# Kernel tuning notes

Measured on AMD Instinct MI355X. Metric: run time of the kernel, lower is better.

Reference implementation:

```python
import jax, jax.numpy as jnp
import numpy as np

N = 100000      # nodes
E = 3200000     # edges (avg degree 32)
F_IN = 512      # input features
H = 16          # hidden (module default)
C = 40          # classes


def _linear_params(key, fan_in, fan_out):
    # torch.nn.Linear default init: U(-1/sqrt(fan_in), 1/sqrt(fan_in))
    k1, k2 = jax.random.split(key)
    lim = 1.0 / np.sqrt(fan_in)
    W = jax.random.uniform(k1, (fan_in, fan_out), jnp.float32, -lim, lim)
    b = jax.random.uniform(k2, (fan_out,), jnp.float32, -lim, lim)
    return W, b


def setup_inputs() -> dict:
    key = jax.random.key(0)
    ks = jax.random.split(key, 8)
    x = jax.random.normal(ks[0], (N, F_IN), jnp.float32)
    edge_index = jax.random.randint(ks[1], (2, E), 0, N, dtype=jnp.int64)
    edge_weight = jax.random.uniform(ks[2], (E,), jnp.float32)
    W_first, b_first = _linear_params(ks[3], F_IN, H)
    W_conv1, b_conv1 = _linear_params(ks[4], H, H)
    W_conv2, b_conv2 = _linear_params(ks[5], H, H)
    W_out, b_out = _linear_params(ks[6], H, C)
    return {
        "x": x, "edge_index": edge_index, "edge_weight": edge_weight,
        "W_first": W_first, "b_first": b_first,
        "W_conv1": W_conv1, "b_conv1": b_conv1,
        "W_conv2": W_conv2, "b_conv2": b_conv2,
        "W_out": W_out, "b_out": b_out,
    }


def _gcn_conv(x, W, b, row, col, ew):
    # PyG GCNConv: h = x @ W; out_i = sum_{(j->i)} norm_e * h_j + b
    # norm_e = deg^-1/2[row] * w_e * deg^-1/2[col], deg from target (col) index,
    # with self-loops (weight 1) already appended to row/col/ew.
    n = x.shape[0]
    deg = jax.ops.segment_sum(ew, col, num_segments=n)
    dinv = jnp.where(deg > 0, jax.lax.rsqrt(deg), 0.0)
    norm = dinv[row] * ew * dinv[col]
    h = x @ W
    out = jax.ops.segment_sum(h[row] * norm[:, None], col, num_segments=n)
    return out + b


def reference(x, edge_index, edge_weight, W_first, b_first,
              W_conv1, b_conv1, W_conv2, b_conv2, W_out, b_out):
    n = x.shape[0]
    # add self-loops once (shared by all conv layers)
    loop = jnp.arange(n, dtype=edge_index.dtype)
    row = jnp.concatenate([edge_index[0], loop])
    col = jnp.concatenate([edge_index[1], loop])
    ew = jnp.concatenate([edge_weight, jnp.ones((n,), edge_weight.dtype)])

    h = jax.nn.relu(x @ W_first + b_first)
    # dropout: eval mode -> identity
    h = jax.nn.relu(_gcn_conv(h, W_conv1, b_conv1, row, col, ew))
    h = jax.nn.relu(_gcn_conv(h, W_conv2, b_conv2, row, col, ew))
    # dropout: eval mode -> identity
    logits = h @ W_out + b_out
    return jax.nn.log_softmax(logits, axis=-1)
```

## Files before the change

kernel.cpp:

```cpp
#include <hip/hip_runtime.h>
#include <hip/hip_bf16.h>
#include <math.h>

#define F_IN 512
#define H 16
#define COUT 40
#define BSH 7
#define BNODES (1 << BSH)
#define SSH 12
#define EPT 64
#define CAP 5376
#define SEG 4096
#define SL 33



__global__ __launch_bounds__(256) void hist_kernel(const int* __restrict__ col,
                                                   int* __restrict__ bcnt, int E, int NBUCK) {
    extern __shared__ int hs[];
    const int t = threadIdx.x;
    for (int i = t; i < NBUCK; i += 256) hs[i] = 0;
    __syncthreads();
    long long e0 = (long long)blockIdx.x * (256 * EPT) + t;
#pragma unroll 4
    for (int k = 0; k < EPT; ++k) {
        long long e = e0 + (long long)k * 256;
        if (e < E) atomicAdd(&hs[col[e] >> BSH], 1);
    }
    __syncthreads();
    for (int i = t; i < NBUCK; i += 256) {
        int h = hs[i];
        if (h > 0) atomicAdd(&bcnt[i], h);
    }
}

__global__ void bscan_kernel(const int* __restrict__ bcnt, int* __restrict__ bbase,
                             int* __restrict__ sbase, int* __restrict__ rowptr,
                             int NBUCK, int nsup, int E, int N) {
    __shared__ int sm[1024];
    int t = threadIdx.x;
    int v = (t < NBUCK) ? bcnt[t] : 0;
    sm[t] = v;
    __syncthreads();
    for (int o = 1; o < 1024; o <<= 1) {
        int u = (t >= o) ? sm[t - o] : 0;
        __syncthreads();
        sm[t] += u;
        __syncthreads();
    }
    if (t < NBUCK) bbase[t] = sm[t] - v;
    if (t == 0) { bbase[NBUCK] = E; rowptr[N] = E; }
    __syncthreads();
    if (t < nsup) {
        int bk = t << (SSH - BSH);
        sbase[t] = (bk < NBUCK) ? (sm[bk] - bcnt[bk]) : E;
    }
    if (t == nsup) sbase[nsup] = E;
}


__global__ __launch_bounds__(256) void scat1_kernel(const int* __restrict__ row,
                                                    const int* __restrict__ col,
                                                    const float* __restrict__ ew,
                                                    const int* __restrict__ sbase,
                                                    int* __restrict__ sfill,
                                                    int2* __restrict__ ptmp, int E, int nsup) {
    __shared__ int2 stg[SEG];
    __shared__ unsigned char sup[SEG];
    __shared__ int cnt[32], base[32];
    const int t = threadIdx.x;
    const int e0 = blockIdx.x * SEG;
    int m = E - e0; if (m > SEG) m = SEG;
    if (t < 32) cnt[t] = 0;
    __syncthreads();
    for (int i = t; i < m; i += 256) {
        int e = e0 + i;
        int c = col[e];
        int s = c >> SSH;
        sup[i] = (unsigned char)s;
        atomicAdd(&cnt[s], 1);
        stg[i] = make_int2(row[e] | ((c & ((1 << SSH) - 1)) << 17), __float_as_int(ew[e]));
    }
    __syncthreads();
    if (t < nsup) {
        int h = cnt[t];
        base[t] = h ? atomicAdd(&sfill[t], h) : 0;
        cnt[t] = 0;
    }
    __syncthreads();
    for (int i = t; i < m; i += 256) {
        int s = sup[i];
        int rk = atomicAdd(&cnt[s], 1);
        ptmp[sbase[s] + base[s] + rk] = stg[i];
    }
}


__global__ __launch_bounds__(256) void scat2_kernel(const int* __restrict__ sbase,
                                                    const int* __restrict__ bbase,
                                                    int* __restrict__ ffill,
                                                    const int2* __restrict__ ptmp,
                                                    int2* __restrict__ packed, int NBUCK) {
    __shared__ int2 stg[SEG];
    __shared__ int cnt[32], base[32];
    const int t = threadIdx.x;
    const int s  = blockIdx.x / SL;
    const int sl = blockIdx.x % SL;
    const int ss = sbase[s];
    const int len = sbase[s + 1] - ss;
    const int lo = ss + (int)((long long)len * sl / SL);
    const int hi = ss + (int)((long long)len * (sl + 1) / SL);
    int m = hi - lo; if (m > SEG) m = SEG;
    if (t < 32) cnt[t] = 0;
    __syncthreads();
    for (int i = t; i < m; i += 256) {
        int2 p = ptmp[lo + i];
        stg[i] = p;
        int bk5 = ((unsigned)p.x >> (17 + BSH)) & 31;
        atomicAdd(&cnt[bk5], 1);
    }
    __syncthreads();
    if (t < 32) {
        int bk = (s << 5) + t;
        int h = cnt[t];
        base[t] = (h && bk < NBUCK) ? atomicAdd(&ffill[bk], h) : 0;
        cnt[t] = 0;
    }
    __syncthreads();
    for (int i = t; i < m; i += 256) {
        int2 p = stg[i];
        int bk5 = ((unsigned)p.x >> (17 + BSH)) & 31;
        int rk = atomicAdd(&cnt[bk5], 1);
        int bk = (s << 5) + bk5;
        packed[bbase[bk] + base[bk5] + rk] = make_int2(p.x & 0xFFFFFF, p.y);
    }
}

__global__ __launch_bounds__(256) void pass2_kernel(const int* __restrict__ bbase,
                                                    int2* __restrict__ packed,
                                                    int* __restrict__ rowptr,
                                                    float* __restrict__ dinv, int N) {
    __shared__ int2  edg[CAP];
    __shared__ int   ncnt[BNODES], nsc[BNODES], nfill[BNODES];
    __shared__ float dsum[BNODES];
    const int t = threadIdx.x;
    const int b = blockIdx.x;
    const int s = bbase[b];
    int cnt = bbase[b + 1] - s;
    if (cnt > CAP) cnt = CAP;

    for (int i = t; i < cnt; i += 256) edg[i] = packed[s + i];
    if (t < BNODES) { ncnt[t] = 0; nfill[t] = 0; dsum[t] = 0.f; }
    __syncthreads();

    for (int i = t; i < cnt; i += 256) {
        int lc = (edg[i].x >> 17) & (BNODES - 1);
        atomicAdd(&ncnt[lc], 1);
        atomicAdd(&dsum[lc], __int_as_float(edg[i].y));
    }
    __syncthreads();
    if (t < BNODES) nsc[t] = ncnt[t];
    __syncthreads();
    for (int o = 1; o < BNODES; o <<= 1) {
        int v = (t < BNODES && t >= o) ? nsc[t - o] : 0;
        __syncthreads();
        if (t < BNODES) nsc[t] += v;
        __syncthreads();
    }
    if (t < BNODES) {
        int n = b * BNODES + t;
        if (n < N) {
            rowptr[n] = s + nsc[t] - ncnt[t];
            dinv[n]   = rsqrtf(1.0f + dsum[t]);
        }
    }
    __syncthreads();
    for (int i = t; i < cnt; i += 256) {
        int lc = (edg[i].x >> 17) & (BNODES - 1);
        int rk = atomicAdd(&nfill[lc], 1);
        packed[s + nsc[lc] - ncnt[lc] + rk] = make_int2(edg[i].x & 0x1FFFF, edg[i].y);
    }
}


#define L1_ROWS 8
#define XS_CH 36
#define XS_ROW (16 * XS_CH)

__global__ __launch_bounds__(256) void l1_kernel(const float* __restrict__ x,
                                                 const float* __restrict__ W,
                                                 const float* __restrict__ b,
                                                 const float* __restrict__ dinv,
                                                 float* __restrict__ g0, int N) {
    __shared__ float xs[L1_ROWS][XS_ROW];
    __shared__ float part[L1_ROWS][256];
    const int t  = threadIdx.x;
    const int o  = t & 15;
    const int fg = t >> 4;

    float Wreg[32];
#pragma unroll
    for (int j = 0; j < 32; ++j) Wreg[j] = W[(fg * 32 + j) * H + o];
    const float bias = b[o];

    const int nbatch = (N + L1_ROWS - 1) / L1_ROWS;
    for (int batch = blockIdx.x; batch < nbatch; batch += gridDim.x) {
        const int row0 = batch * L1_ROWS;
#pragma unroll
        for (int bq = 0; bq < 4; ++bq) {
            int L  = bq * 256 + t;
            int rl = L >> 7;
            int f4 = L & 127;
            int r  = row0 + rl;
            float4 v = make_float4(0.f, 0.f, 0.f, 0.f);
            if (r < N) v = *(const float4*)&x[(size_t)r * F_IN + f4 * 4];
            int fgs = f4 >> 3, j4 = f4 & 7;
            *(float4*)&xs[rl][fgs * XS_CH + j4 * 4] = v;
        }
        __syncthreads();

        float acc[L1_ROWS];
#pragma unroll
        for (int r = 0; r < L1_ROWS; ++r) acc[r] = 0.f;
#pragma unroll
        for (int j4 = 0; j4 < 8; ++j4) {
#pragma unroll
            for (int r = 0; r < L1_ROWS; ++r) {
                float4 xv = *(const float4*)&xs[r][fg * XS_CH + j4 * 4];
                acc[r] = fmaf(xv.x, Wreg[j4 * 4 + 0], acc[r]);
                acc[r] = fmaf(xv.y, Wreg[j4 * 4 + 1], acc[r]);
                acc[r] = fmaf(xv.z, Wreg[j4 * 4 + 2], acc[r]);
                acc[r] = fmaf(xv.w, Wreg[j4 * 4 + 3], acc[r]);
            }
        }
#pragma unroll
        for (int r = 0; r < L1_ROWS; ++r) part[r][fg * 16 + o] = acc[r];
        __syncthreads();

        if (t < 128) {
            int r = t >> 4, oo = t & 15;
            float s = 0.f;
#pragma unroll
            for (int g = 0; g < 16; ++g) s += part[r][g * 16 + oo];
            s = fmaxf(s + bias, 0.f);
            int rr = row0 + r;
            if (rr < N) g0[(size_t)rr * H + oo] = s * dinv[rr];
        }
        __syncthreads();
    }
}


template<bool LAST>
__global__ __launch_bounds__(256) void conv_kernel(const int* __restrict__ rowptr,
                                                   const int2* __restrict__ packed,
                                                   const float* __restrict__ g_in,
                                                   const float* __restrict__ dinv,
                                                   const float* __restrict__ Wc,
                                                   const float* __restrict__ bc,
                                                   const float* __restrict__ Wo,
                                                   const float* __restrict__ bo,
                                                   float* __restrict__ out, int N) {
    __shared__ float Wcs[H * H];
    __shared__ float bcs[H];
    __shared__ float Wos[H * 48];
    __shared__ float bos[48];
    const int tt = threadIdx.x;
    if (tt < H * H) Wcs[tt] = Wc[tt];
    if (tt < H) bcs[tt] = bc[tt];
    if (LAST) {
        for (int i = tt; i < H * 48; i += 256) {
            int f = i / 48, c = i % 48;
            Wos[i] = (c < COUT) ? Wo[f * COUT + c] : 0.f;
        }
        if (tt < 48) bos[tt] = (tt < COUT) ? bo[tt] : 0.f;
    }
    __syncthreads();

    int t = blockIdx.x * 256 + tt;
    int n = t >> 4, o = t & 15;
    if (n >= N) return;

    int s = rowptr[n], e = rowptr[n + 1];
    float acc = g_in[(size_t)n * H + o];
    int i = s;
    for (; i + 4 <= e; i += 4) {
        int2 p0 = packed[i],     p1 = packed[i + 1];
        int2 p2 = packed[i + 2], p3 = packed[i + 3];
        float h0 = g_in[(size_t)p0.x * H + o];
        float h1 = g_in[(size_t)p1.x * H + o];
        float h2 = g_in[(size_t)p2.x * H + o];
        float h3 = g_in[(size_t)p3.x * H + o];
        acc = fmaf(__int_as_float(p0.y), h0, acc);
        acc = fmaf(__int_as_float(p1.y), h1, acc);
        acc = fmaf(__int_as_float(p2.y), h2, acc);
        acc = fmaf(__int_as_float(p3.y), h3, acc);
    }
    for (; i < e; ++i) {
        int2 p = packed[i];
        acc = fmaf(__int_as_float(p.y), g_in[(size_t)p.x * H + o], acc);
    }
    const float di = dinv[n];
    const float y = di * acc;

    float h = bcs[o];
#pragma unroll
    for (int f = 0; f < H; ++f) {
        float yf = __shfl(y, f, 16);
        h = fmaf(yf, Wcs[f * H + o], h);
    }
    h = fmaxf(h, 0.f);

    if (!LAST) {
        out[(size_t)n * H + o] = di * h;
    } else {
        float l0 = bos[o], l1 = bos[o + 16], l2 = bos[o + 32];
#pragma unroll
        for (int f = 0; f < H; ++f) {
            float hf = __shfl(h, f, 16);
            l0 = fmaf(hf, Wos[f * 48 + o], l0);
            l1 = fmaf(hf, Wos[f * 48 + o + 16], l1);
            l2 = fmaf(hf, Wos[f * 48 + o + 32], l2);
        }
        float m = fmaxf(l0, l1);
        if (o < 8) m = fmaxf(m, l2);
#pragma unroll
        for (int d = 1; d < 16; d <<= 1) m = fmaxf(m, __shfl_xor(m, d, 16));
        float sx = __expf(l0 - m) + __expf(l1 - m) + ((o < 8) ? __expf(l2 - m) : 0.f);
#pragma unroll
        for (int d = 1; d < 16; d <<= 1) sx += __shfl_xor(sx, d, 16);
        float lse = m + __logf(sx);
        out[(size_t)n * COUT + o]      = l0 - lse;
        out[(size_t)n * COUT + o + 16] = l1 - lse;
        if (o < 8) out[(size_t)n * COUT + o + 32] = l2 - lse;
    }
}


extern "C" void kernel_launch(void* const* d_in, const int* in_sizes, int n_in,
                              void* d_out, int out_size, void* d_ws, size_t ws_size,
                              hipStream_t stream) {
    const float* x       = (const float*)d_in[0];
    const int*   ei      = (const int*)d_in[1];
    const float* ew      = (const float*)d_in[2];
    const float* W_first = (const float*)d_in[3];
    const float* b_first = (const float*)d_in[4];
    const float* W_c1    = (const float*)d_in[5];
    const float* b_c1    = (const float*)d_in[6];
    const float* W_c2    = (const float*)d_in[7];
    const float* b_c2    = (const float*)d_in[8];
    const float* W_o     = (const float*)d_in[9];
    const float* b_o     = (const float*)d_in[10];

    const int N = in_sizes[0] / F_IN;
    const int E = in_sizes[2];
    const int NBUCK = (N + BNODES - 1) >> BSH;
    const int NSUP  = ((N - 1) >> SSH) + 1;
    const int HB    = (E + 256 * EPT - 1) / (256 * EPT);
    const int SB    = (E + SEG - 1) / SEG;

    const int* row = ei;
    const int* col = ei + E;

    char* wsb = (char*)d_ws;
    int*   bcnt   = (int*)wsb;                  wsb += (size_t)NBUCK * 4;
    int*   sfill  = (int*)wsb;                  wsb += (size_t)32 * 4;
    int*   ffill  = (int*)wsb;                  wsb += (size_t)NBUCK * 4;
    int*   bbase  = (int*)wsb;                  wsb += (size_t)(NBUCK + 1) * 4;
    int*   sbase  = (int*)wsb;                  wsb += (size_t)(NSUP + 1) * 4;
    int*   rowptr = (int*)wsb;                  wsb += (size_t)(N + 1) * 4;
    float* dinv   = (float*)wsb;                wsb += (size_t)N * 4;
    int2*  packed = (int2*)wsb;                 wsb += (size_t)E * 8;
    int2*  ptmp   = (int2*)wsb;                 wsb += (size_t)E * 8;
    float* g0     = (float*)ptmp;
    float* g1     = (float*)ptmp + (size_t)N * H;

    hipMemsetAsync(bcnt, 0, (size_t)(NBUCK * 2 + 32) * 4, stream);

    hist_kernel<<<HB, 256, NBUCK * 4, stream>>>(col, bcnt, E, NBUCK);
    bscan_kernel<<<1, 1024, 0, stream>>>(bcnt, bbase, sbase, rowptr, NBUCK, NSUP, E, N);
    scat1_kernel<<<SB, 256, 0, stream>>>(row, col, ew, sbase, sfill, ptmp, E, NSUP);
    scat2_kernel<<<NSUP * SL, 256, 0, stream>>>(sbase, bbase, ffill, ptmp, packed, NBUCK);
    pass2_kernel<<<NBUCK, 256, 0, stream>>>(bbase, packed, rowptr, dinv, N);

    l1_kernel<<<1024, 256, 0, stream>>>(x, W_first, b_first, dinv, g0, N);

    conv_kernel<false><<<(N * 16 + 255) / 256, 256, 0, stream>>>(
        rowptr, packed, g0, dinv, W_c1, b_c1, nullptr, nullptr, g1, N);

    conv_kernel<true><<<(N * 16 + 255) / 256, 256, 0, stream>>>(
        rowptr, packed, g1, dinv, W_c2, b_c2, W_o, b_o, (float*)d_out, N);
}
```

Baseline: 573.3 us.

## Restructure first-layer GEMV to float4 output tiles with two-stage reduction

The first dense layer (512->16) kernel now has each thread hold a 4-output by 8-input weight tile in float4 registers, with 4 rows per batch instead of 8. Partial sums are reduced through a padded shared buffer in two stages, then bias, ReLU and dinv are applied and written as float4. The aim is wider shared-memory and register use and fewer reduction steps per output. The cost is an extra barrier per batch, and with half the rows per batch the weights are reused less per x load.

```diff
diff --git a/kernel.cpp b/kernel.cpp
--- a/kernel.cpp
+++ b/kernel.cpp
@@ -183,68 +183,96 @@
 }
 
 
-#define L1_ROWS 8
-#define XS_CH 36
-#define XS_ROW (16 * XS_CH)
+#define L1_ROWS 4
+
+#define ACC4(xc, wv) \
+    s.x = fmaf(xc, wv.x, s.x); s.y = fmaf(xc, wv.y, s.y); \
+    s.z = fmaf(xc, wv.z, s.z); s.w = fmaf(xc, wv.w, s.w);
 
 __global__ __launch_bounds__(256) void l1_kernel(const float* __restrict__ x,
                                                  const float* __restrict__ W,
                                                  const float* __restrict__ b,
                                                  const float* __restrict__ dinv,
                                                  float* __restrict__ g0, int N) {
-    __shared__ float xs[L1_ROWS][XS_ROW];
-    __shared__ float part[L1_ROWS][256];
-    const int t  = threadIdx.x;
-    const int o  = t & 15;
-    const int fg = t >> 4;
-
-    float Wreg[32];
-#pragma unroll
-    for (int j = 0; j < 32; ++j) Wreg[j] = W[(fg * 32 + j) * H + o];
-    const float bias = b[o];
+    __shared__ float xs[L1_ROWS][F_IN];
+    __shared__ float P[64 * 68];
+    __shared__ float Q[128 * 4];
+    __shared__ float bl[16];
+    const int t = threadIdx.x;
+    const int w = t >> 6;
+    const int l = t & 63;
+
+    if (t < 16) bl[t] = b[t];
+
+    float4 Wr[8];
+#pragma unroll
+    for (int j = 0; j < 4; ++j) {
+        Wr[j]     = *(const float4*)&W[(4 * l + j) * H + 4 * w];
+        Wr[4 + j] = *(const float4*)&W[(256 + 4 * l + j) * H + 4 * w];
+    }
 
     const int nbatch = (N + L1_ROWS - 1) / L1_ROWS;
     for (int batch = blockIdx.x; batch < nbatch; batch += gridDim.x) {
         const int row0 = batch * L1_ROWS;
 #pragma unroll
-        for (int bq = 0; bq < 4; ++bq) {
+        for (int bq = 0; bq < 2; ++bq) {
             int L  = bq * 256 + t;
             int rl = L >> 7;
             int f4 = L & 127;
             int r  = row0 + rl;
             float4 v = make_float4(0.f, 0.f, 0.f, 0.f);
             if (r < N) v = *(const float4*)&x[(size_t)r * F_IN + f4 * 4];
-            int fgs = f4 >> 3, j4 = f4 & 7;
-            *(float4*)&xs[rl][fgs * XS_CH + j4 * 4] = v;
-        }
-        __syncthreads();
-
-        float acc[L1_ROWS];
-#pragma unroll
-        for (int r = 0; r < L1_ROWS; ++r) acc[r] = 0.f;
-#pragma unroll
-        for (int j4 = 0; j4 < 8; ++j4) {
-#pragma unroll
-            for (int r = 0; r < L1_ROWS; ++r) {
-                float4 xv = *(const float4*)&xs[r][fg * XS_CH + j4 * 4];
-                acc[r] = fmaf(xv.x, Wreg[j4 * 4 + 0], acc[r]);
-                acc[r] = fmaf(xv.y, Wreg[j4 * 4 + 1], acc[r]);
-                acc[r] = fmaf(xv.z, Wreg[j4 * 4 + 2], acc[r]);
-                acc[r] = fmaf(xv.w, Wreg[j4 * 4 + 3], acc[r]);
+            *(float4*)&xs[rl][f4 * 4] = v;
+        }
+        __syncthreads();
+
+        float4 acc[L1_ROWS];
+#pragma unroll
+        for (int r = 0; r < L1_ROWS; ++r) {
+            const float4 x0 = *(const float4*)&xs[r][4 * l];
+            const float4 x1 = *(const float4*)&xs[r][256 + 4 * l];
+            float4 s = make_float4(0.f, 0.f, 0.f, 0.f);
+            ACC4(x0.x, Wr[0]); ACC4(x0.y, Wr[1]); ACC4(x0.z, Wr[2]); ACC4(x0.w, Wr[3]);
+            ACC4(x1.x, Wr[4]); ACC4(x1.y, Wr[5]); ACC4(x1.z, Wr[6]); ACC4(x1.w, Wr[7]);
+            acc[r] = s;
+        }
+#pragma unroll
+        for (int r = 0; r < L1_ROWS; ++r)
+            *(float4*)&P[l * 68 + r * 16 + w * 4] = acc[r];
+        __syncthreads();
+
+        if (t < 128) {
+            const int r8 = t >> 5;
+            const int oq = (t >> 3) & 3;
+            const int f8 = t & 7;
+            float4 s = make_float4(0.f, 0.f, 0.f, 0.f);
+#pragma unroll
+            for (int i = 0; i < 8; ++i) {
+                const float4 p = *(const float4*)&P[(f8 * 8 + i) * 68 + r8 * 16 + oq * 4];
+                s.x += p.x; s.y += p.y; s.z += p.z; s.w += p.w;
             }
-        }
-#pragma unroll
-        for (int r = 0; r < L1_ROWS; ++r) part[r][fg * 16 + o] = acc[r];
-        __syncthreads();
-
-        if (t < 128) {
-            int r = t >> 4, oo = t & 15;
-            float s = 0.f;
-#pragma unroll
-            for (int g = 0; g < 16; ++g) s += part[r][g * 16 + oo];
-            s = fmaxf(s + bias, 0.f);
-            int rr = row0 + r;
-            if (rr < N) g0[(size_t)rr * H + oo] = s * dinv[rr];
+            *(float4*)&Q[t * 4] = s;
+        }
+        __syncthreads();
+
+        if (t < 16) {
+            const int r8 = t >> 2, oq = t & 3;
+            float4 s = make_float4(0.f, 0.f, 0.f, 0.f);
+#pragma unroll
+            for (int f = 0; f < 8; ++f) {
+                const float4 q = *(const float4*)&Q[((r8 * 4 + oq) * 8 + f) * 4];
+                s.x += q.x; s.y += q.y; s.z += q.z; s.w += q.w;
+            }
+            int rr = row0 + r8;
+            if (rr < N) {
+                const float di = dinv[rr];
+                float4 o4;
+                o4.x = fmaxf(s.x + bl[oq * 4 + 0], 0.f) * di;
+                o4.y = fmaxf(s.y + bl[oq * 4 + 1], 0.f) * di;
+                o4.z = fmaxf(s.z + bl[oq * 4 + 2], 0.f) * di;
+                o4.w = fmaxf(s.w + bl[oq * 4 + 3], 0.f) * di;
+                *(float4*)&g0[(size_t)rr * H + oq * 4] = o4;
+            }
         }
         __syncthreads();
     }
```

Measured after the change: 576.1 us. Within noise of the previous version (+0.5%).
